# Performance work log

Measured on AMD Instinct MI355X. Metric: run time of the kernel, lower is better.

## Reference

```python
import jax, jax.numpy as jnp
import numpy as np

N = 50000      # nodes
E = 800000     # edges (avg degree 16)
EMB = 128      # emb_dim
NF = 7         # x_features
EF = 5         # edge_features
L = 5          # num_layer
BN_EPS = 1e-5


def setup_inputs() -> dict:
    key = jax.random.key(0)
    ks = jax.random.split(key, 12)
    s = 0.05
    return {
        "x": jax.random.normal(ks[0], (N, NF), jnp.float32),
        "edge_attr": jax.random.normal(ks[1], (E, EF), jnp.float32),
        "edge_index": jax.random.randint(ks[2], (2, E), 0, N, dtype=jnp.int32),
        "W_x": jax.random.normal(ks[3], (NF, EMB), jnp.float32) * s,
        "b_x": jax.random.normal(ks[4], (NF, EMB), jnp.float32) * s,
        "W_e": jax.random.normal(ks[5], (L, EF, EMB), jnp.float32) * s,
        "b_e": jax.random.normal(ks[6], (L, EF, EMB), jnp.float32) * s,
        # per-layer GIN update MLP: Linear(EMB,2EMB)-ReLU-Linear(2EMB,EMB)
        "W1": jax.random.normal(ks[7], (L, EMB, 2 * EMB), jnp.float32) * s,
        "b1": jnp.zeros((L, 2 * EMB), jnp.float32),
        "W2": jax.random.normal(ks[8], (L, 2 * EMB, EMB), jnp.float32) * s,
        "b2": jnp.zeros((L, EMB), jnp.float32),
        # per-layer BatchNorm1d affine params
        "gamma": jnp.ones((L, EMB), jnp.float32),
        "beta": jnp.zeros((L, EMB), jnp.float32),
    }


def reference(x, edge_attr, W_x, b_x, W_e, b_e, W1, b1, W2, b2, gamma, beta, edge_index):
    src, dst = edge_index[0], edge_index[1]
    # initial node embedding: sum of 7 Linear(1,EMB) applied per column == x @ W_x + sum(biases)
    h = x @ W_x + b_x.sum(axis=0)  # [N, EMB]
    for l in range(L):
        # edge embeddings: sum of EF Linear(1,EMB) over edge_attr columns
        e_emb = edge_attr @ W_e[l] + b_e[l].sum(axis=0)  # [E, EMB]
        sl_emb = b_e[l].sum(axis=0)  # self-loop edges have zero attr -> bias sum
        # message = x_j + edge_emb, aggr = add (scatter over dst); self loops add h + sl_emb
        msg = h[src] + e_emb                                        # [E, EMB]
        agg = jax.ops.segment_sum(msg, dst, num_segments=N) + h + sl_emb  # [N, EMB]
        # GIN update MLP
        z = jax.nn.relu(agg @ W1[l] + b1[l]) @ W2[l] + b2[l]        # [N, EMB]
        # BatchNorm1d (training-mode batch stats, biased variance)
        mu = z.mean(axis=0)
        var = z.var(axis=0)
        z = (z - mu) * jax.lax.rsqrt(var + BN_EPS) * gamma[l] + beta[l]
        # ELU on all but last layer; dropout is identity at drop_ratio=0; JK='last'
        h = jax.nn.elu(z) if l < L - 1 else z
    return h
```

## Files before the change

kernel.cpp:

```cpp
#include <hip/hip_runtime.h>
#include <math.h>

#define NN 50000
#define NE 800000
#define EMB 128
#define HID 256
#define NF 7
#define EF 5
#define NL 5
#define BN_EPS 1e-5f
#define NREP 32
#define SCAN_B 196
#define NBUCK 49

typedef _Float16 f16x8 __attribute__((ext_vector_type(8)));
typedef _Float16 f16x2 __attribute__((ext_vector_type(2)));
typedef __attribute__((ext_vector_type(4))) float f32x4;

__device__ inline unsigned pkh2(float a, float b) {
    union { unsigned v; _Float16 h[2]; } x;
    x.h[0] = (_Float16)a; x.h[1] = (_Float16)b;
    return x.v;
}
__device__ inline float2 uph2(unsigned u) {
    union { unsigned v; _Float16 h[2]; } x; x.v = u;
    return make_float2((float)x.h[0], (float)x.h[1]);
}
__device__ inline unsigned short f2h_bits(float f) {
    _Float16 h = (_Float16)f;
    return __builtin_bit_cast(unsigned short, h);
}
__device__ inline float h_bits2f(unsigned short b) {
    return (float)__builtin_bit_cast(_Float16, b);
}
__device__ inline f16x2 as_h2(unsigned u) { return __builtin_bit_cast(f16x2, u); }

__global__ void k_prep(const float* __restrict__ b_x, const float* __restrict__ b_e,
                       float* __restrict__ bsum_x, float* __restrict__ bsum_e,
                       int* __restrict__ counts, int* __restrict__ cursor) {
    int tid = threadIdx.x;
    if (blockIdx.x == 0 && tid < EMB) {
        float s = 0.f;
        for (int f = 0; f < NF; ++f) s += b_x[f * EMB + tid];
        bsum_x[tid] = s;
        for (int l = 0; l < NL; ++l) {
            float se = 0.f;
            for (int f = 0; f < EF; ++f) se += b_e[(l * EF + f) * EMB + tid];
            bsum_e[l * EMB + tid] = se;
        }
    }
    int gid = blockIdx.x * blockDim.x + tid;
    int stride = gridDim.x * blockDim.x;
    for (int i = gid; i < NN; i += stride) { counts[i] = 0; cursor[i] = 0; }
}

__global__ void k_prepw(const float* __restrict__ W1, const float* __restrict__ W2,
                        unsigned short* __restrict__ W1ph, unsigned short* __restrict__ W1pl,
                        unsigned short* __restrict__ W2ph, unsigned short* __restrict__ W2pl) {
    const int TOT = NL * EMB * HID;
    int gid = blockIdx.x * blockDim.x + threadIdx.x;
    if (gid < TOT) {
        int l = gid / (EMB * HID);
        int r = gid % (EMB * HID);
        int w = r >> 13;
        int rem = r & 8191;
        int h2 = rem >> 11;
        int rem2 = rem & 2047;
        int kk = rem2 >> 9;
        int rem3 = rem2 & 511;
        int lane = rem3 >> 3;
        int j = rem3 & 7;
        int hc = w * 64 + h2 * 16 + (lane & 15);
        int k = kk * 32 + (lane >> 4) * 8 + j;
        float wv = W1[((size_t)l * EMB + k) * HID + hc];
        unsigned short hi = f2h_bits(wv);
        W1ph[gid] = hi;
        W1pl[gid] = f2h_bits(wv - h_bits2f(hi));
    } else if (gid < 2 * TOT) {
        int g = gid - TOT;
        int l = g / (EMB * HID);
        int r = g % (EMB * HID);
        int w = r >> 13;
        int rem = r & 8191;
        int o2 = rem >> 12;
        int rem2 = rem & 4095;
        int kk = rem2 >> 9;
        int rem3 = rem2 & 511;
        int lane = rem3 >> 3;
        int j = rem3 & 7;
        int oc = w * 32 + o2 * 16 + (lane & 15);
        int k2 = kk * 32 + (lane >> 4) * 8 + j;
        float wv = W2[((size_t)l * HID + k2) * EMB + oc];
        unsigned short hi = f2h_bits(wv);
        W2ph[g] = hi;
        W2pl[g] = f2h_bits(wv - h_bits2f(hi));
    }
}

__global__ void k_init(const float* __restrict__ x, const float* __restrict__ W_x,
                       const float* __restrict__ bsum_x, unsigned short* __restrict__ h16) {
    int gid = blockIdx.x * blockDim.x + threadIdx.x;
    int v = gid >> 5;
    if (v >= NN) return;
    int c = (gid & 31) << 2;
    float4 acc = *(const float4*)(bsum_x + c);
    #pragma unroll
    for (int f = 0; f < NF; ++f) {
        float xv = x[(size_t)v * NF + f];
        float4 w = *(const float4*)(W_x + f * EMB + c);
        acc.x += xv * w.x; acc.y += xv * w.y; acc.z += xv * w.z; acc.w += xv * w.w;
    }
    uint2 p = make_uint2(pkh2(acc.x, acc.y), pkh2(acc.z, acc.w));
    *(uint2*)(h16 + (size_t)v * EMB + c) = p;
}

__global__ void k_hist(const int* __restrict__ dst, int* __restrict__ counts) {
    int e = blockIdx.x * blockDim.x + threadIdx.x;
    if (e < NE) atomicAdd(&counts[dst[e]], 1);
}

__global__ void k_scan1(const int* __restrict__ counts, int* __restrict__ bsum) {
    int tid = threadIdx.x;
    int i = blockIdx.x * 256 + tid;
    int v = (i < NN) ? counts[i] : 0;
    #pragma unroll
    for (int off = 1; off < 64; off <<= 1) v += __shfl_xor(v, off, 64);
    __shared__ int ws[4];
    if ((tid & 63) == 0) ws[tid >> 6] = v;
    __syncthreads();
    if (tid == 0) bsum[blockIdx.x] = ws[0] + ws[1] + ws[2] + ws[3];
}

__global__ void k_scan2(const int* __restrict__ bsum, int* __restrict__ bpre,
                        int* __restrict__ row_start) {
    int tid = threadIdx.x;
    int x = (tid < SCAN_B) ? bsum[tid] : 0;
    int lane = tid & 63, wv = tid >> 6;
    int v = x;
    #pragma unroll
    for (int off = 1; off < 64; off <<= 1) {
        int t = __shfl_up(v, off, 64);
        if (lane >= off) v += t;
    }
    __shared__ int wsum[4];
    if (lane == 63) wsum[wv] = v;
    __syncthreads();
    int woff = 0;
    #pragma unroll
    for (int w = 0; w < 4; ++w) if (w < wv) woff += wsum[w];
    int incl = v + woff;
    if (tid < SCAN_B) bpre[tid] = incl - x;
    if (tid == 255) row_start[NN] = incl;
}

__global__ void k_scan3(const int* __restrict__ counts, const int* __restrict__ bpre,
                        int* __restrict__ row_start, int* __restrict__ bcur) {
    int tid = threadIdx.x;
    int i = blockIdx.x * 256 + tid;
    int x = (i < NN) ? counts[i] : 0;
    int lane = tid & 63, wv = tid >> 6;
    int v = x;
    #pragma unroll
    for (int off = 1; off < 64; off <<= 1) {
        int t = __shfl_up(v, off, 64);
        if (lane >= off) v += t;
    }
    __shared__ int wsum[4];
    if (lane == 63) wsum[wv] = v;
    __syncthreads();
    int woff = 0;
    #pragma unroll
    for (int w = 0; w < 4; ++w) if (w < wv) woff += wsum[w];
    if (i < NN) {
        int rs = bpre[blockIdx.x] + v + woff - x;
        row_start[i] = rs;
        if ((i & 1023) == 0) bcur[i >> 10] = rs;
    }
}

#define BPB 2048
__global__ __launch_bounds__(256) void k_bucket(
        const int* __restrict__ src, const int* __restrict__ dst,
        const float* __restrict__ edge_attr,
        int* __restrict__ bcur, uint4* __restrict__ grouped) {
    __shared__ int lcnt[NBUCK];
    __shared__ int lbase[NBUCK];
    int tid = threadIdx.x;
    if (tid < NBUCK) lcnt[tid] = 0;
    __syncthreads();
    int base = blockIdx.x * BPB;
    int b_[8];
    int d_[8];
    #pragma unroll
    for (int k = 0; k < 8; ++k) {
        int e = base + k * 256 + tid;
        if (e < NE) {
            int d = dst[e];
            d_[k] = d;
            b_[k] = d >> 10;
            atomicAdd(&lcnt[b_[k]], 1);
        } else b_[k] = -1;
    }
    __syncthreads();
    if (tid < NBUCK) {
        lbase[tid] = (lcnt[tid] > 0) ? atomicAdd(&bcur[tid], lcnt[tid]) : 0;
        lcnt[tid] = 0;
    }
    __syncthreads();
    #pragma unroll
    for (int k = 0; k < 8; ++k) {
        int e = base + k * 256 + tid;
        if (e < NE) {
            int b = b_[k];
            int off = lbase[b] + atomicAdd(&lcnt[b], 1);
            const float* ea = edge_attr + (size_t)e * EF;
            uint4 pk;
            pk.x = (unsigned)src[e];
            pk.y = pkh2(ea[0], ea[1]);
            pk.z = pkh2(ea[2], ea[3]);
            pk.w = (unsigned)f2h_bits(ea[4]) | ((unsigned)d_[k] << 16);
            grouped[off] = pk;
        }
    }
}

__global__ void k_place(const uint4* __restrict__ grouped,
                        const int* __restrict__ row_start, int* __restrict__ cursor,
                        uint4* __restrict__ sorted_pk) {
    int e = blockIdx.x * blockDim.x + threadIdx.x;
    if (e >= NE) return;
    uint4 pk = grouped[e];
    int d = (int)(pk.w >> 16);
    int pos = atomicAdd(&cursor[d], 1);
    sorted_pk[row_start[d] + pos] = pk;
}

__global__ void k_esum(const uint4* __restrict__ sorted_pk,
                       const int* __restrict__ row_start,
                       float* __restrict__ attsum, int* __restrict__ sorted_srcc) {
    int v = blockIdx.x * blockDim.x + threadIdx.x;
    if (v >= NN) return;
    int e0 = row_start[v], e1 = row_start[v + 1];
    float s0 = 0.f, s1 = 0.f, s2 = 0.f, s3 = 0.f, s4 = 0.f;
    for (int e = e0; e < e1; ++e) {
        uint4 pk = sorted_pk[e];
        sorted_srcc[e] = (int)pk.x;
        float2 a01 = uph2(pk.y), a23 = uph2(pk.z);
        s0 += a01.x; s1 += a01.y; s2 += a23.x; s3 += a23.y;
        s4 += h_bits2f((unsigned short)(pk.w & 0xffffu));
    }
    float* o = attsum + (size_t)v * 8;
    *(float4*)(o) = make_float4(s0, s1, s2, s3);
    *(float4*)(o + 4) = make_float4(s4, (float)(e1 - e0), 0.f, 0.f);
}

__global__ __launch_bounds__(256) void k_agg(
        const unsigned short* __restrict__ h16, const int* __restrict__ sorted_srcc,
        const float* __restrict__ attsum,
        const float* __restrict__ W_e_l, const float* __restrict__ bsum_e_l,
        const int* __restrict__ row_start,
        unsigned short* __restrict__ agg16, float* __restrict__ stats) {
    int tid = threadIdx.x;
    if (blockIdx.x < NREP) stats[blockIdx.x * 2 * EMB + tid] = 0.f;
    int gid = blockIdx.x * 256 + tid;
    int v = gid >> 6;
    if (v >= NN) return;
    int c = (gid & 63) << 1;
    float2 we0 = *(const float2*)(W_e_l + 0 * EMB + c);
    float2 we1 = *(const float2*)(W_e_l + 1 * EMB + c);
    float2 we2 = *(const float2*)(W_e_l + 2 * EMB + c);
    float2 we3 = *(const float2*)(W_e_l + 3 * EMB + c);
    float2 we4 = *(const float2*)(W_e_l + 4 * EMB + c);
    float2 bs = *(const float2*)(bsum_e_l + c);
    float2 hv = uph2(*(const unsigned*)(h16 + (size_t)v * EMB + c));
    const float* at = attsum + (size_t)v * 8;
    float4 a03 = *(const float4*)(at);
    float2 a45 = *(const float2*)(at + 4);
    float ax = hv.x + (a45.y + 1.f) * bs.x
             + a03.x*we0.x + a03.y*we1.x + a03.z*we2.x + a03.w*we3.x + a45.x*we4.x;
    float ay = hv.y + (a45.y + 1.f) * bs.y
             + a03.x*we0.y + a03.y*we1.y + a03.z*we2.y + a03.w*we3.y + a45.x*we4.y;
    int e0 = row_start[v], e1 = row_start[v + 1];
    int e = e0;
    for (; e + 16 <= e1; e += 16) {
        int s0 = __builtin_amdgcn_readfirstlane(sorted_srcc[e + 0]);
        int s1 = __builtin_amdgcn_readfirstlane(sorted_srcc[e + 1]);
        int s2 = __builtin_amdgcn_readfirstlane(sorted_srcc[e + 2]);
        int s3 = __builtin_amdgcn_readfirstlane(sorted_srcc[e + 3]);
        int s4 = __builtin_amdgcn_readfirstlane(sorted_srcc[e + 4]);
        int s5 = __builtin_amdgcn_readfirstlane(sorted_srcc[e + 5]);
        int s6 = __builtin_amdgcn_readfirstlane(sorted_srcc[e + 6]);
        int s7 = __builtin_amdgcn_readfirstlane(sorted_srcc[e + 7]);
        int s8 = __builtin_amdgcn_readfirstlane(sorted_srcc[e + 8]);
        int s9 = __builtin_amdgcn_readfirstlane(sorted_srcc[e + 9]);
        int sa = __builtin_amdgcn_readfirstlane(sorted_srcc[e + 10]);
        int sb = __builtin_amdgcn_readfirstlane(sorted_srcc[e + 11]);
        int sc = __builtin_amdgcn_readfirstlane(sorted_srcc[e + 12]);
        int sd = __builtin_amdgcn_readfirstlane(sorted_srcc[e + 13]);
        int se = __builtin_amdgcn_readfirstlane(sorted_srcc[e + 14]);
        int sf = __builtin_amdgcn_readfirstlane(sorted_srcc[e + 15]);
        unsigned u0 = *(const unsigned*)(h16 + (size_t)s0 * EMB + c);
        unsigned u1 = *(const unsigned*)(h16 + (size_t)s1 * EMB + c);
        unsigned u2 = *(const unsigned*)(h16 + (size_t)s2 * EMB + c);
        unsigned u3 = *(const unsigned*)(h16 + (size_t)s3 * EMB + c);
        unsigned u4 = *(const unsigned*)(h16 + (size_t)s4 * EMB + c);
        unsigned u5 = *(const unsigned*)(h16 + (size_t)s5 * EMB + c);
        unsigned u6 = *(const unsigned*)(h16 + (size_t)s6 * EMB + c);
        unsigned u7 = *(const unsigned*)(h16 + (size_t)s7 * EMB + c);
        unsigned u8 = *(const unsigned*)(h16 + (size_t)s8 * EMB + c);
        unsigned u9 = *(const unsigned*)(h16 + (size_t)s9 * EMB + c);
        unsigned ua = *(const unsigned*)(h16 + (size_t)sa * EMB + c);
        unsigned ub = *(const unsigned*)(h16 + (size_t)sb * EMB + c);
        unsigned uc = *(const unsigned*)(h16 + (size_t)sc * EMB + c);
        unsigned ud = *(const unsigned*)(h16 + (size_t)sd * EMB + c);
        unsigned ue = *(const unsigned*)(h16 + (size_t)se * EMB + c);
        unsigned uf = *(const unsigned*)(h16 + (size_t)sf * EMB + c);
        f16x2 pA = ((as_h2(u0) + as_h2(u1)) + (as_h2(u2) + as_h2(u3)))
                 + ((as_h2(u4) + as_h2(u5)) + (as_h2(u6) + as_h2(u7)));
        f16x2 pB = ((as_h2(u8) + as_h2(u9)) + (as_h2(ua) + as_h2(ub)))
                 + ((as_h2(uc) + as_h2(ud)) + (as_h2(ue) + as_h2(uf)));
        ax += (float)pA.x + (float)pB.x;
        ay += (float)pA.y + (float)pB.y;
    }
    for (; e + 8 <= e1; e += 8) {
        int s0 = __builtin_amdgcn_readfirstlane(sorted_srcc[e + 0]);
        int s1 = __builtin_amdgcn_readfirstlane(sorted_srcc[e + 1]);
        int s2 = __builtin_amdgcn_readfirstlane(sorted_srcc[e + 2]);
        int s3 = __builtin_amdgcn_readfirstlane(sorted_srcc[e + 3]);
        int s4 = __builtin_amdgcn_readfirstlane(sorted_srcc[e + 4]);
        int s5 = __builtin_amdgcn_readfirstlane(sorted_srcc[e + 5]);
        int s6 = __builtin_amdgcn_readfirstlane(sorted_srcc[e + 6]);
        int s7 = __builtin_amdgcn_readfirstlane(sorted_srcc[e + 7]);
        unsigned u0 = *(const unsigned*)(h16 + (size_t)s0 * EMB + c);
        unsigned u1 = *(const unsigned*)(h16 + (size_t)s1 * EMB + c);
        unsigned u2 = *(const unsigned*)(h16 + (size_t)s2 * EMB + c);
        unsigned u3 = *(const unsigned*)(h16 + (size_t)s3 * EMB + c);
        unsigned u4 = *(const unsigned*)(h16 + (size_t)s4 * EMB + c);
        unsigned u5 = *(const unsigned*)(h16 + (size_t)s5 * EMB + c);
        unsigned u6 = *(const unsigned*)(h16 + (size_t)s6 * EMB + c);
        unsigned u7 = *(const unsigned*)(h16 + (size_t)s7 * EMB + c);
        f16x2 p07 = ((as_h2(u0) + as_h2(u1)) + (as_h2(u2) + as_h2(u3)))
                  + ((as_h2(u4) + as_h2(u5)) + (as_h2(u6) + as_h2(u7)));
        ax += (float)p07.x;
        ay += (float)p07.y;
    }
    for (; e < e1; ++e) {
        int s = __builtin_amdgcn_readfirstlane(sorted_srcc[e]);
        float2 hs = uph2(*(const unsigned*)(h16 + (size_t)s * EMB + c));
        ax += hs.x;
        ay += hs.y;
    }
    *(unsigned*)(agg16 + (size_t)v * EMB + c) = pkh2(ax, ay);
}

__global__ __launch_bounds__(256) void k_mlp(
        const unsigned short* __restrict__ agg16,
        const unsigned short* __restrict__ W1ph, const unsigned short* __restrict__ W1pl,
        const float* __restrict__ b1_l,
        const unsigned short* __restrict__ W2ph, const unsigned short* __restrict__ W2pl,
        const float* __restrict__ b2_l,
        unsigned short* __restrict__ z16, float* __restrict__ stats) {
    __shared__ unsigned short A16[64][136];
    __shared__ unsigned short Hid16[64][264];
    int tid = threadIdx.x;
    int r0 = blockIdx.x * 64;
    int rep = blockIdx.x & (NREP - 1);
    #pragma unroll
    for (int it = 0; it < 4; ++it) {
        int idx = it * 256 + tid;
        int row = idx >> 4;
        int cb = (idx & 15) * 8;
        int grow = r0 + row;
        uint4 val = make_uint4(0u, 0u, 0u, 0u);
        if (grow < NN) val = *(const uint4*)(agg16 + (size_t)grow * EMB + cb);
        *(uint4*)(&A16[row][cb]) = val;
    }
    __syncthreads();
    int wave = tid >> 6, lane = tid & 63;
    int l16 = lane & 15, quad = lane >> 4;
    {
        f16x8 af[4][4];
        #pragma unroll
        for (int nt = 0; nt < 4; ++nt)
            #pragma unroll
            for (int kk = 0; kk < 4; ++kk)
                af[nt][kk] = *(const f16x8*)(&A16[nt * 16 + l16][kk * 32 + quad * 8]);
        #pragma unroll
        for (int h2 = 0; h2 < 4; ++h2) {
            f16x8 whf[4], wlf[4];
            #pragma unroll
            for (int kk = 0; kk < 4; ++kk) {
                size_t off = ((((size_t)(wave * 4 + h2) * 4) + kk) * 64 + lane) * 8;
                whf[kk] = *(const f16x8*)(W1ph + off);
                wlf[kk] = *(const f16x8*)(W1pl + off);
            }
            float4 bv = *(const float4*)(b1_l + wave * 64 + h2 * 16 + quad * 4);
            f32x4 bias = {bv.x, bv.y, bv.z, bv.w};
            #pragma unroll
            for (int nt = 0; nt < 4; ++nt) {
                f32x4 acc = bias;
                #pragma unroll
                for (int kk = 0; kk < 4; ++kk)
                    acc = __builtin_amdgcn_mfma_f32_16x16x32_f16(whf[kk], af[nt][kk], acc, 0, 0, 0);
                #pragma unroll
                for (int kk = 0; kk < 4; ++kk)
                    acc = __builtin_amdgcn_mfma_f32_16x16x32_f16(wlf[kk], af[nt][kk], acc, 0, 0, 0);
                uint2 p;
                p.x = pkh2(fmaxf(acc[0], 0.f), fmaxf(acc[1], 0.f));
                p.y = pkh2(fmaxf(acc[2], 0.f), fmaxf(acc[3], 0.f));
                int col = wave * 64 + h2 * 16 + quad * 4;
                *(uint2*)(&Hid16[nt * 16 + l16][col]) = p;
            }
        }
    }
    __syncthreads();
    float ss[2][4] = {}, sq[2][4] = {};
    #pragma unroll
    for (int o2 = 0; o2 < 2; ++o2) {
        f16x8 w2h[8], w2l[8];
        #pragma unroll
        for (int kk = 0; kk < 8; ++kk) {
            size_t off = ((((size_t)(wave * 2 + o2) * 8) + kk) * 64 + lane) * 8;
            w2h[kk] = *(const f16x8*)(W2ph + off);
            w2l[kk] = *(const f16x8*)(W2pl + off);
        }
        float4 bv = *(const float4*)(b2_l + wave * 32 + o2 * 16 + quad * 4);
        f32x4 bias = {bv.x, bv.y, bv.z, bv.w};
        #pragma unroll
        for (int nt = 0; nt < 4; ++nt) {
            f16x8 hf[8];
            #pragma unroll
            for (int kk = 0; kk < 8; ++kk)
                hf[kk] = *(const f16x8*)(&Hid16[nt * 16 + l16][kk * 32 + quad * 8]);
            f32x4 acc = bias;
            #pragma unroll
            for (int kk = 0; kk < 8; ++kk)
                acc = __builtin_amdgcn_mfma_f32_16x16x32_f16(w2h[kk], hf[kk], acc, 0, 0, 0);
            #pragma unroll
            for (int kk = 0; kk < 8; ++kk)
                acc = __builtin_amdgcn_mfma_f32_16x16x32_f16(w2l[kk], hf[kk], acc, 0, 0, 0);
            int node = r0 + nt * 16 + l16;
            if (node < NN) {
                uint2 p = make_uint2(pkh2(acc[0], acc[1]), pkh2(acc[2], acc[3]));
                *(uint2*)(z16 + (size_t)node * EMB + wave * 32 + o2 * 16 + quad * 4) = p;
                #pragma unroll
                for (int r = 0; r < 4; ++r) {
                    ss[o2][r] += acc[r];
                    sq[o2][r] += acc[r] * acc[r];
                }
            }
        }
    }
    #pragma unroll
    for (int o2 = 0; o2 < 2; ++o2)
        #pragma unroll
        for (int r = 0; r < 4; ++r) {
            float s = ss[o2][r], q = sq[o2][r];
            #pragma unroll
            for (int m = 1; m < 16; m <<= 1) {
                s += __shfl_xor(s, m, 64);
                q += __shfl_xor(q, m, 64);
            }
            if (l16 == 0) {
                int oc = wave * 32 + o2 * 16 + quad * 4 + r;
                atomicAdd(&stats[rep * 2 * EMB + oc], s);
                atomicAdd(&stats[rep * 2 * EMB + EMB + oc], q);
            }
        }
}

__global__ void k_bnscale(const float* __restrict__ stats,
                          const float* __restrict__ gamma_l, const float* __restrict__ beta_l,
                          float* __restrict__ scsh) {
    int tid = threadIdx.x;
    float s = 0.f, q = 0.f;
    #pragma unroll
    for (int r = 0; r < NREP; ++r) {
        s += stats[r * 2 * EMB + tid];
        q += stats[r * 2 * EMB + EMB + tid];
    }
    float mu = s * (1.f / NN);
    float var = q * (1.f / NN) - mu * mu;
    float sf = gamma_l[tid] * rsqrtf(var + BN_EPS);
    scsh[tid] = sf;
    scsh[EMB + tid] = beta_l[tid] - mu * sf;
}

__global__ void k_bn(const unsigned short* __restrict__ z16, const float* __restrict__ scsh,
                     unsigned short* __restrict__ h16, float* __restrict__ fout, int last) {
    __shared__ float sc[EMB], sh[EMB];
    int tid = threadIdx.x;
    if (tid < EMB) {
        sc[tid] = scsh[tid];
        sh[tid] = scsh[EMB + tid];
    }
    __syncthreads();
    int gid = blockIdx.x * blockDim.x + tid;
    if (gid >= NN * EMB / 4) return;
    int c = (gid & 31) << 2;
    uint2 zp = *(const uint2*)(z16 + (size_t)gid * 4);
    float2 z01 = uph2(zp.x), z23 = uph2(zp.y);
    float o0 = z01.x * sc[c + 0] + sh[c + 0];
    float o1 = z01.y * sc[c + 1] + sh[c + 1];
    float o2 = z23.x * sc[c + 2] + sh[c + 2];
    float o3 = z23.y * sc[c + 3] + sh[c + 3];
    if (!last) {
        o0 = (o0 > 0.f) ? o0 : (__expf(o0) - 1.f);
        o1 = (o1 > 0.f) ? o1 : (__expf(o1) - 1.f);
        o2 = (o2 > 0.f) ? o2 : (__expf(o2) - 1.f);
        o3 = (o3 > 0.f) ? o3 : (__expf(o3) - 1.f);
        uint2 p = make_uint2(pkh2(o0, o1), pkh2(o2, o3));
        *(uint2*)(h16 + (size_t)gid * 4) = p;
    } else {
        *(float4*)(fout + (size_t)gid * 4) = make_float4(o0, o1, o2, o3);
    }
}

extern "C" void kernel_launch(void* const* d_in, const int* in_sizes, int n_in,
                              void* d_out, int out_size, void* d_ws, size_t ws_size,
                              hipStream_t stream) {
    const float* x         = (const float*)d_in[0];
    const float* edge_attr = (const float*)d_in[1];
    const int*   edge_idx  = (const int*)d_in[2];
    const float* W_x   = (const float*)d_in[3];
    const float* b_x   = (const float*)d_in[4];
    const float* W_e   = (const float*)d_in[5];
    const float* b_e   = (const float*)d_in[6];
    const float* W1    = (const float*)d_in[7];
    const float* b1    = (const float*)d_in[8];
    const float* W2    = (const float*)d_in[9];
    const float* b2    = (const float*)d_in[10];
    const float* gamma = (const float*)d_in[11];
    const float* beta  = (const float*)d_in[12];
    float* fout = (float*)d_out;

    const int* src = edge_idx;
    const int* dst = edge_idx + NE;

    char* p = (char*)d_ws;
    auto alloc = [&](size_t bytes) { char* q = p; p += (bytes + 255) & ~(size_t)255; return q; };
    unsigned short* h16  = (unsigned short*)alloc((size_t)NN * EMB * 2);
    unsigned short* z16  = (unsigned short*)alloc((size_t)NN * EMB * 2);
    unsigned short* agg16 = (unsigned short*)alloc((size_t)NN * EMB * 2);
    unsigned short* W1ph = (unsigned short*)alloc((size_t)NL * HID * EMB * 2);
    unsigned short* W1pl = (unsigned short*)alloc((size_t)NL * HID * EMB * 2);
    unsigned short* W2ph = (unsigned short*)alloc((size_t)NL * EMB * HID * 2);
    unsigned short* W2pl = (unsigned short*)alloc((size_t)NL * EMB * HID * 2);
    int*   row_start  = (int*)alloc((NN + 1) * sizeof(int));
    int*   counts     = (int*)alloc(NN * sizeof(int));
    int*   cursor     = (int*)alloc(NN * sizeof(int));
    uint4* grouped    = (uint4*)alloc((size_t)NE * sizeof(uint4));
    uint4* sorted_pk  = (uint4*)alloc((size_t)NE * sizeof(uint4));
    int*   sorted_srcc= (int*)alloc((size_t)NE * sizeof(int));
    float* attsum     = (float*)alloc((size_t)NN * 8 * sizeof(float));
    int*   bsum       = (int*)alloc(SCAN_B * sizeof(int));
    int*   bpre       = (int*)alloc(SCAN_B * sizeof(int));
    int*   bcur       = (int*)alloc(NBUCK * sizeof(int));
    float* stats      = (float*)alloc((size_t)NREP * 2 * EMB * sizeof(float));
    float* scsh       = (float*)alloc(2 * EMB * sizeof(float));
    float* bsum_x     = (float*)alloc(EMB * sizeof(float));
    float* bsum_e     = (float*)alloc(NL * EMB * sizeof(float));

    k_prep<<<256, 256, 0, stream>>>(b_x, b_e, bsum_x, bsum_e, counts, cursor);
    k_prepw<<<(2 * NL * EMB * HID + 255) / 256, 256, 0, stream>>>(W1, W2, W1ph, W1pl, W2ph, W2pl);
    k_init<<<(NN * 32 + 255) / 256, 256, 0, stream>>>(x, W_x, bsum_x, h16);
    k_hist<<<(NE + 255) / 256, 256, 0, stream>>>(dst, counts);
    k_scan1<<<SCAN_B, 256, 0, stream>>>(counts, bsum);
    k_scan2<<<1, 256, 0, stream>>>(bsum, bpre, row_start);
    k_scan3<<<SCAN_B, 256, 0, stream>>>(counts, bpre, row_start, bcur);
    k_bucket<<<(NE + BPB - 1) / BPB, 256, 0, stream>>>(src, dst, edge_attr, bcur, grouped);
    k_place<<<(NE + 255) / 256, 256, 0, stream>>>(grouped, row_start, cursor, sorted_pk);
    k_esum<<<SCAN_B, 256, 0, stream>>>(sorted_pk, row_start, attsum, sorted_srcc);
    const int AGG_GRID = (NN * 64 + 255) / 256;
    for (int l = 0; l < NL; ++l) {
        k_agg<<<AGG_GRID, 256, 0, stream>>>(
            h16, sorted_srcc, attsum,
            W_e + (size_t)l * EF * EMB, bsum_e + l * EMB, row_start,
            agg16, stats);
        k_mlp<<<(NN + 63) / 64, 256, 0, stream>>>(
            agg16,
            W1ph + (size_t)l * HID * EMB, W1pl + (size_t)l * HID * EMB, b1 + (size_t)l * HID,
            W2ph + (size_t)l * EMB * HID, W2pl + (size_t)l * EMB * HID, b2 + (size_t)l * EMB,
            z16, stats);
        k_bnscale<<<1, 128, 0, stream>>>(stats, gamma + l * EMB, beta + l * EMB, scsh);
        k_bn<<<(NN * EMB / 4 + 255) / 256, 256, 0, stream>>>(
            z16, scsh, h16, fout, (l == NL - 1) ? 1 : 0);
    }
}
```

Measured before the change: 572.2 us.

## Fuse neighbor aggregation into MLP kernel and merge BN scale into BN apply

```diff
diff --git a/kernel.cpp b/kernel.cpp
--- a/kernel.cpp
+++ b/kernel.cpp
@@ -37,7 +37,8 @@
 
 __global__ void k_prep(const float* __restrict__ b_x, const float* __restrict__ b_e,
                        float* __restrict__ bsum_x, float* __restrict__ bsum_e,
-                       int* __restrict__ counts, int* __restrict__ cursor) {
+                       int* __restrict__ counts, int* __restrict__ cursor,
+                       float* __restrict__ stats) {
     int tid = threadIdx.x;
     if (blockIdx.x == 0 && tid < EMB) {
         float s = 0.f;
@@ -52,6 +53,8 @@
     int gid = blockIdx.x * blockDim.x + tid;
     int stride = gridDim.x * blockDim.x;
     for (int i = gid; i < NN; i += stride) { counts[i] = 0; cursor[i] = 0; }
+    const int STOT = NL * NREP * 2 * EMB;
+    for (int i = gid; i < STOT; i += stride) stats[i] = 0.f;
 }
 
 __global__ void k_prepw(const float* __restrict__ W1, const float* __restrict__ W2,
@@ -254,129 +257,119 @@
     *(float4*)(o + 4) = make_float4(s4, (float)(e1 - e0), 0.f, 0.f);
 }
 
-__global__ __launch_bounds__(256) void k_agg(
+__global__ __launch_bounds__(256) void k_fused(
         const unsigned short* __restrict__ h16, const int* __restrict__ sorted_srcc,
         const float* __restrict__ attsum,
         const float* __restrict__ W_e_l, const float* __restrict__ bsum_e_l,
         const int* __restrict__ row_start,
-        unsigned short* __restrict__ agg16, float* __restrict__ stats) {
-    int tid = threadIdx.x;
-    if (blockIdx.x < NREP) stats[blockIdx.x * 2 * EMB + tid] = 0.f;
-    int gid = blockIdx.x * 256 + tid;
-    int v = gid >> 6;
-    if (v >= NN) return;
-    int c = (gid & 63) << 1;
-    float2 we0 = *(const float2*)(W_e_l + 0 * EMB + c);
-    float2 we1 = *(const float2*)(W_e_l + 1 * EMB + c);
-    float2 we2 = *(const float2*)(W_e_l + 2 * EMB + c);
-    float2 we3 = *(const float2*)(W_e_l + 3 * EMB + c);
-    float2 we4 = *(const float2*)(W_e_l + 4 * EMB + c);
-    float2 bs = *(const float2*)(bsum_e_l + c);
-    float2 hv = uph2(*(const unsigned*)(h16 + (size_t)v * EMB + c));
-    const float* at = attsum + (size_t)v * 8;
-    float4 a03 = *(const float4*)(at);
-    float2 a45 = *(const float2*)(at + 4);
-    float ax = hv.x + (a45.y + 1.f) * bs.x
-             + a03.x*we0.x + a03.y*we1.x + a03.z*we2.x + a03.w*we3.x + a45.x*we4.x;
-    float ay = hv.y + (a45.y + 1.f) * bs.y
-             + a03.x*we0.y + a03.y*we1.y + a03.z*we2.y + a03.w*we3.y + a45.x*we4.y;
-    int e0 = row_start[v], e1 = row_start[v + 1];
-    int e = e0;
-    for (; e + 16 <= e1; e += 16) {
-        int s0 = __builtin_amdgcn_readfirstlane(sorted_srcc[e + 0]);
-        int s1 = __builtin_amdgcn_readfirstlane(sorted_srcc[e + 1]);
-        int s2 = __builtin_amdgcn_readfirstlane(sorted_srcc[e + 2]);
-        int s3 = __builtin_amdgcn_readfirstlane(sorted_srcc[e + 3]);
-        int s4 = __builtin_amdgcn_readfirstlane(sorted_srcc[e + 4]);
-        int s5 = __builtin_amdgcn_readfirstlane(sorted_srcc[e + 5]);
-        int s6 = __builtin_amdgcn_readfirstlane(sorted_srcc[e + 6]);
-        int s7 = __builtin_amdgcn_readfirstlane(sorted_srcc[e + 7]);
-        int s8 = __builtin_amdgcn_readfirstlane(sorted_srcc[e + 8]);
-        int s9 = __builtin_amdgcn_readfirstlane(sorted_srcc[e + 9]);
-        int sa = __builtin_amdgcn_readfirstlane(sorted_srcc[e + 10]);
-        int sb = __builtin_amdgcn_readfirstlane(sorted_srcc[e + 11]);
-        int sc = __builtin_amdgcn_readfirstlane(sorted_srcc[e + 12]);
-        int sd = __builtin_amdgcn_readfirstlane(sorted_srcc[e + 13]);
-        int se = __builtin_amdgcn_readfirstlane(sorted_srcc[e + 14]);
-        int sf = __builtin_amdgcn_readfirstlane(sorted_srcc[e + 15]);
-        unsigned u0 = *(const unsigned*)(h16 + (size_t)s0 * EMB + c);
-        unsigned u1 = *(const unsigned*)(h16 + (size_t)s1 * EMB + c);
-        unsigned u2 = *(const unsigned*)(h16 + (size_t)s2 * EMB + c);
-        unsigned u3 = *(const unsigned*)(h16 + (size_t)s3 * EMB + c);
-        unsigned u4 = *(const unsigned*)(h16 + (size_t)s4 * EMB + c);
-        unsigned u5 = *(const unsigned*)(h16 + (size_t)s5 * EMB + c);
-        unsigned u6 = *(const unsigned*)(h16 + (size_t)s6 * EMB + c);
-        unsigned u7 = *(const unsigned*)(h16 + (size_t)s7 * EMB + c);
-        unsigned u8 = *(const unsigned*)(h16 + (size_t)s8 * EMB + c);
-        unsigned u9 = *(const unsigned*)(h16 + (size_t)s9 * EMB + c);
-        unsigned ua = *(const unsigned*)(h16 + (size_t)sa * EMB + c);
-        unsigned ub = *(const unsigned*)(h16 + (size_t)sb * EMB + c);
-        unsigned uc = *(const unsigned*)(h16 + (size_t)sc * EMB + c);
-        unsigned ud = *(const unsigned*)(h16 + (size_t)sd * EMB + c);
-        unsigned ue = *(const unsigned*)(h16 + (size_t)se * EMB + c);
-        unsigned uf = *(const unsigned*)(h16 + (size_t)sf * EMB + c);
-        f16x2 pA = ((as_h2(u0) + as_h2(u1)) + (as_h2(u2) + as_h2(u3)))
-                 + ((as_h2(u4) + as_h2(u5)) + (as_h2(u6) + as_h2(u7)));
-        f16x2 pB = ((as_h2(u8) + as_h2(u9)) + (as_h2(ua) + as_h2(ub)))
-                 + ((as_h2(uc) + as_h2(ud)) + (as_h2(ue) + as_h2(uf)));
-        ax += (float)pA.x + (float)pB.x;
-        ay += (float)pA.y + (float)pB.y;
-    }
-    for (; e + 8 <= e1; e += 8) {
-        int s0 = __builtin_amdgcn_readfirstlane(sorted_srcc[e + 0]);
-        int s1 = __builtin_amdgcn_readfirstlane(sorted_srcc[e + 1]);
-        int s2 = __builtin_amdgcn_readfirstlane(sorted_srcc[e + 2]);
-        int s3 = __builtin_amdgcn_readfirstlane(sorted_srcc[e + 3]);
-        int s4 = __builtin_amdgcn_readfirstlane(sorted_srcc[e + 4]);
-        int s5 = __builtin_amdgcn_readfirstlane(sorted_srcc[e + 5]);
-        int s6 = __builtin_amdgcn_readfirstlane(sorted_srcc[e + 6]);
-        int s7 = __builtin_amdgcn_readfirstlane(sorted_srcc[e + 7]);
-        unsigned u0 = *(const unsigned*)(h16 + (size_t)s0 * EMB + c);
-        unsigned u1 = *(const unsigned*)(h16 + (size_t)s1 * EMB + c);
-        unsigned u2 = *(const unsigned*)(h16 + (size_t)s2 * EMB + c);
-        unsigned u3 = *(const unsigned*)(h16 + (size_t)s3 * EMB + c);
-        unsigned u4 = *(const unsigned*)(h16 + (size_t)s4 * EMB + c);
-        unsigned u5 = *(const unsigned*)(h16 + (size_t)s5 * EMB + c);
-        unsigned u6 = *(const unsigned*)(h16 + (size_t)s6 * EMB + c);
-        unsigned u7 = *(const unsigned*)(h16 + (size_t)s7 * EMB + c);
-        f16x2 p07 = ((as_h2(u0) + as_h2(u1)) + (as_h2(u2) + as_h2(u3)))
-                  + ((as_h2(u4) + as_h2(u5)) + (as_h2(u6) + as_h2(u7)));
-        ax += (float)p07.x;
-        ay += (float)p07.y;
-    }
-    for (; e < e1; ++e) {
-        int s = __builtin_amdgcn_readfirstlane(sorted_srcc[e]);
-        float2 hs = uph2(*(const unsigned*)(h16 + (size_t)s * EMB + c));
-        ax += hs.x;
-        ay += hs.y;
-    }
-    *(unsigned*)(agg16 + (size_t)v * EMB + c) = pkh2(ax, ay);
-}
-
-__global__ __launch_bounds__(256) void k_mlp(
-        const unsigned short* __restrict__ agg16,
         const unsigned short* __restrict__ W1ph, const unsigned short* __restrict__ W1pl,
         const float* __restrict__ b1_l,
         const unsigned short* __restrict__ W2ph, const unsigned short* __restrict__ W2pl,
         const float* __restrict__ b2_l,
-        unsigned short* __restrict__ z16, float* __restrict__ stats) {
+        unsigned short* __restrict__ z16, float* __restrict__ stats_l) {
     __shared__ unsigned short A16[64][136];
     __shared__ unsigned short Hid16[64][264];
     int tid = threadIdx.x;
+    int wave = tid >> 6, lane = tid & 63;
     int r0 = blockIdx.x * 64;
     int rep = blockIdx.x & (NREP - 1);
-    #pragma unroll
-    for (int it = 0; it < 4; ++it) {
-        int idx = it * 256 + tid;
-        int row = idx >> 4;
-        int cb = (idx & 15) * 8;
-        int grow = r0 + row;
-        uint4 val = make_uint4(0u, 0u, 0u, 0u);
-        if (grow < NN) val = *(const uint4*)(agg16 + (size_t)grow * EMB + cb);
-        *(uint4*)(&A16[row][cb]) = val;
-    }
-    __syncthreads();
-    int wave = tid >> 6, lane = tid & 63;
+
+    {
+        int c = lane << 1;
+        float2 we0 = *(const float2*)(W_e_l + 0 * EMB + c);
+        float2 we1 = *(const float2*)(W_e_l + 1 * EMB + c);
+        float2 we2 = *(const float2*)(W_e_l + 2 * EMB + c);
+        float2 we3 = *(const float2*)(W_e_l + 3 * EMB + c);
+        float2 we4 = *(const float2*)(W_e_l + 4 * EMB + c);
+        float2 bs = *(const float2*)(bsum_e_l + c);
+        for (int i = 0; i < 16; ++i) {
+            int v = r0 + wave * 16 + i;
+            unsigned out = 0u;
+            if (v < NN) {
+                float2 hv = uph2(*(const unsigned*)(h16 + (size_t)v * EMB + c));
+                const float* at = attsum + (size_t)v * 8;
+                float4 a03 = *(const float4*)(at);
+                float2 a45 = *(const float2*)(at + 4);
+                float ax = hv.x + (a45.y + 1.f) * bs.x
+                         + a03.x*we0.x + a03.y*we1.x + a03.z*we2.x + a03.w*we3.x + a45.x*we4.x;
+                float ay = hv.y + (a45.y + 1.f) * bs.y
+                         + a03.x*we0.y + a03.y*we1.y + a03.z*we2.y + a03.w*we3.y + a45.x*we4.y;
+                int e0 = row_start[v], e1 = row_start[v + 1];
+                int e = e0;
+                for (; e + 16 <= e1; e += 16) {
+                    int s0 = __builtin_amdgcn_readfirstlane(sorted_srcc[e + 0]);
+                    int s1 = __builtin_amdgcn_readfirstlane(sorted_srcc[e + 1]);
+                    int s2 = __builtin_amdgcn_readfirstlane(sorted_srcc[e + 2]);
+                    int s3 = __builtin_amdgcn_readfirstlane(sorted_srcc[e + 3]);
+                    int s4 = __builtin_amdgcn_readfirstlane(sorted_srcc[e + 4]);
+                    int s5 = __builtin_amdgcn_readfirstlane(sorted_srcc[e + 5]);
+                    int s6 = __builtin_amdgcn_readfirstlane(sorted_srcc[e + 6]);
+                    int s7 = __builtin_amdgcn_readfirstlane(sorted_srcc[e + 7]);
+                    int s8 = __builtin_amdgcn_readfirstlane(sorted_srcc[e + 8]);
+                    int s9 = __builtin_amdgcn_readfirstlane(sorted_srcc[e + 9]);
+                    int sa = __builtin_amdgcn_readfirstlane(sorted_srcc[e + 10]);
+                    int sb = __builtin_amdgcn_readfirstlane(sorted_srcc[e + 11]);
+                    int sc = __builtin_amdgcn_readfirstlane(sorted_srcc[e + 12]);
+                    int sd = __builtin_amdgcn_readfirstlane(sorted_srcc[e + 13]);
+                    int se = __builtin_amdgcn_readfirstlane(sorted_srcc[e + 14]);
+                    int sf = __builtin_amdgcn_readfirstlane(sorted_srcc[e + 15]);
+                    unsigned u0 = *(const unsigned*)(h16 + (size_t)s0 * EMB + c);
+                    unsigned u1 = *(const unsigned*)(h16 + (size_t)s1 * EMB + c);
+                    unsigned u2 = *(const unsigned*)(h16 + (size_t)s2 * EMB + c);
+                    unsigned u3 = *(const unsigned*)(h16 + (size_t)s3 * EMB + c);
+                    unsigned u4 = *(const unsigned*)(h16 + (size_t)s4 * EMB + c);
+                    unsigned u5 = *(const unsigned*)(h16 + (size_t)s5 * EMB + c);
+                    unsigned u6 = *(const unsigned*)(h16 + (size_t)s6 * EMB + c);
+                    unsigned u7 = *(const unsigned*)(h16 + (size_t)s7 * EMB + c);
+                    unsigned u8 = *(const unsigned*)(h16 + (size_t)s8 * EMB + c);
+                    unsigned u9 = *(const unsigned*)(h16 + (size_t)s9 * EMB + c);
+                    unsigned ua = *(const unsigned*)(h16 + (size_t)sa * EMB + c);
+                    unsigned ub = *(const unsigned*)(h16 + (size_t)sb * EMB + c);
+                    unsigned uc = *(const unsigned*)(h16 + (size_t)sc * EMB + c);
+                    unsigned ud = *(const unsigned*)(h16 + (size_t)sd * EMB + c);
+                    unsigned ue = *(const unsigned*)(h16 + (size_t)se * EMB + c);
+                    unsigned uf = *(const unsigned*)(h16 + (size_t)sf * EMB + c);
+                    f16x2 pA = ((as_h2(u0) + as_h2(u1)) + (as_h2(u2) + as_h2(u3)))
+                             + ((as_h2(u4) + as_h2(u5)) + (as_h2(u6) + as_h2(u7)));
+                    f16x2 pB = ((as_h2(u8) + as_h2(u9)) + (as_h2(ua) + as_h2(ub)))
+                             + ((as_h2(uc) + as_h2(ud)) + (as_h2(ue) + as_h2(uf)));
+                    ax += (float)pA.x + (float)pB.x;
+                    ay += (float)pA.y + (float)pB.y;
+                }
+                for (; e + 8 <= e1; e += 8) {
+                    int s0 = __builtin_amdgcn_readfirstlane(sorted_srcc[e + 0]);
+                    int s1 = __builtin_amdgcn_readfirstlane(sorted_srcc[e + 1]);
+                    int s2 = __builtin_amdgcn_readfirstlane(sorted_srcc[e + 2]);
+                    int s3 = __builtin_amdgcn_readfirstlane(sorted_srcc[e + 3]);
+                    int s4 = __builtin_amdgcn_readfirstlane(sorted_srcc[e + 4]);
+                    int s5 = __builtin_amdgcn_readfirstlane(sorted_srcc[e + 5]);
+                    int s6 = __builtin_amdgcn_readfirstlane(sorted_srcc[e + 6]);
+                    int s7 = __builtin_amdgcn_readfirstlane(sorted_srcc[e + 7]);
+                    unsigned u0 = *(const unsigned*)(h16 + (size_t)s0 * EMB + c);
+                    unsigned u1 = *(const unsigned*)(h16 + (size_t)s1 * EMB + c);
+                    unsigned u2 = *(const unsigned*)(h16 + (size_t)s2 * EMB + c);
+                    unsigned u3 = *(const unsigned*)(h16 + (size_t)s3 * EMB + c);
+                    unsigned u4 = *(const unsigned*)(h16 + (size_t)s4 * EMB + c);
+                    unsigned u5 = *(const unsigned*)(h16 + (size_t)s5 * EMB + c);
+                    unsigned u6 = *(const unsigned*)(h16 + (size_t)s6 * EMB + c);
+                    unsigned u7 = *(const unsigned*)(h16 + (size_t)s7 * EMB + c);
+                    f16x2 p07 = ((as_h2(u0) + as_h2(u1)) + (as_h2(u2) + as_h2(u3)))
+                              + ((as_h2(u4) + as_h2(u5)) + (as_h2(u6) + as_h2(u7)));
+                    ax += (float)p07.x;
+                    ay += (float)p07.y;
+                }
+                for (; e < e1; ++e) {
+                    int s = __builtin_amdgcn_readfirstlane(sorted_srcc[e]);
+                    float2 hs = uph2(*(const unsigned*)(h16 + (size_t)s * EMB + c));
+                    ax += hs.x;
+                    ay += hs.y;
+                }
+                out = pkh2(ax, ay);
+            }
+            *(unsigned*)(&A16[wave * 16 + i][c]) = out;
+        }
+    }
+    __syncthreads();
     int l16 = lane & 15, quad = lane >> 4;
     {
         f16x8 af[4][4];
@@ -463,56 +456,54 @@
             }
             if (l16 == 0) {
                 int oc = wave * 32 + o2 * 16 + quad * 4 + r;
-                atomicAdd(&stats[rep * 2 * EMB + oc], s);
-                atomicAdd(&stats[rep * 2 * EMB + EMB + oc], q);
+                atomicAdd(&stats_l[rep * 2 * EMB + oc], s);
+                atomicAdd(&stats_l[rep * 2 * EMB + EMB + oc], q);
             }
         }
 }
 
-__global__ void k_bnscale(const float* __restrict__ stats,
+__global__ void k_bnfused(const float* __restrict__ stats_l,
                           const float* __restrict__ gamma_l, const float* __restrict__ beta_l,
-                          float* __restrict__ scsh) {
-    int tid = threadIdx.x;
-    float s = 0.f, q = 0.f;
-    #pragma unroll
-    for (int r = 0; r < NREP; ++r) {
-        s += stats[r * 2 * EMB + tid];
-        q += stats[r * 2 * EMB + EMB + tid];
-    }
-    float mu = s * (1.f / NN);
-    float var = q * (1.f / NN) - mu * mu;
-    float sf = gamma_l[tid] * rsqrtf(var + BN_EPS);
-    scsh[tid] = sf;
-    scsh[EMB + tid] = beta_l[tid] - mu * sf;
-}
-
-__global__ void k_bn(const unsigned short* __restrict__ z16, const float* __restrict__ scsh,
-                     unsigned short* __restrict__ h16, float* __restrict__ fout, int last) {
+                          const unsigned short* __restrict__ z16,
+                          unsigned short* __restrict__ h16, float* __restrict__ fout, int last) {
+    __shared__ float red[2 * EMB];
     __shared__ float sc[EMB], sh[EMB];
     int tid = threadIdx.x;
+    {
+        float acc = 0.f;
+        #pragma unroll
+        for (int r = 0; r < NREP; ++r) acc += stats_l[r * 2 * EMB + tid];
+        red[tid] = acc;
+    }
+    __syncthreads();
     if (tid < EMB) {
-        sc[tid] = scsh[tid];
-        sh[tid] = scsh[EMB + tid];
-    }
-    __syncthreads();
-    int gid = blockIdx.x * blockDim.x + tid;
-    if (gid >= NN * EMB / 4) return;
-    int c = (gid & 31) << 2;
-    uint2 zp = *(const uint2*)(z16 + (size_t)gid * 4);
-    float2 z01 = uph2(zp.x), z23 = uph2(zp.y);
-    float o0 = z01.x * sc[c + 0] + sh[c + 0];
-    float o1 = z01.y * sc[c + 1] + sh[c + 1];
-    float o2 = z23.x * sc[c + 2] + sh[c + 2];
-    float o3 = z23.y * sc[c + 3] + sh[c + 3];
-    if (!last) {
-        o0 = (o0 > 0.f) ? o0 : (__expf(o0) - 1.f);
-        o1 = (o1 > 0.f) ? o1 : (__expf(o1) - 1.f);
-        o2 = (o2 > 0.f) ? o2 : (__expf(o2) - 1.f);
-        o3 = (o3 > 0.f) ? o3 : (__expf(o3) - 1.f);
-        uint2 p = make_uint2(pkh2(o0, o1), pkh2(o2, o3));
-        *(uint2*)(h16 + (size_t)gid * 4) = p;
-    } else {
-        *(float4*)(fout + (size_t)gid * 4) = make_float4(o0, o1, o2, o3);
+        float s = red[tid], q = red[EMB + tid];
+        float mu = s * (1.f / NN);
+        float var = q * (1.f / NN) - mu * mu;
+        float sf = gamma_l[tid] * rsqrtf(var + BN_EPS);
+        sc[tid] = sf;
+        sh[tid] = beta_l[tid] - mu * sf;
+    }
+    __syncthreads();
+    const int TOT = NN * EMB / 4;
+    for (int gid = blockIdx.x * 256 + tid; gid < TOT; gid += gridDim.x * 256) {
+        int c = (gid & 31) << 2;
+        uint2 zp = *(const uint2*)(z16 + (size_t)gid * 4);
+        float2 z01 = uph2(zp.x), z23 = uph2(zp.y);
+        float o0 = z01.x * sc[c + 0] + sh[c + 0];
+        float o1 = z01.y * sc[c + 1] + sh[c + 1];
+        float o2 = z23.x * sc[c + 2] + sh[c + 2];
+        float o3 = z23.y * sc[c + 3] + sh[c + 3];
+        if (!last) {
+            o0 = (o0 > 0.f) ? o0 : (__expf(o0) - 1.f);
+            o1 = (o1 > 0.f) ? o1 : (__expf(o1) - 1.f);
+            o2 = (o2 > 0.f) ? o2 : (__expf(o2) - 1.f);
+            o3 = (o3 > 0.f) ? o3 : (__expf(o3) - 1.f);
+            uint2 p = make_uint2(pkh2(o0, o1), pkh2(o2, o3));
+            *(uint2*)(h16 + (size_t)gid * 4) = p;
+        } else {
+            *(float4*)(fout + (size_t)gid * 4) = make_float4(o0, o1, o2, o3);
+        }
     }
 }
 
@@ -541,7 +532,6 @@
     auto alloc = [&](size_t bytes) { char* q = p; p += (bytes + 255) & ~(size_t)255; return q; };
     unsigned short* h16  = (unsigned short*)alloc((size_t)NN * EMB * 2);
     unsigned short* z16  = (unsigned short*)alloc((size_t)NN * EMB * 2);
-    unsigned short* agg16 = (unsigned short*)alloc((size_t)NN * EMB * 2);
     unsigned short* W1ph = (unsigned short*)alloc((size_t)NL * HID * EMB * 2);
     unsigned short* W1pl = (unsigned short*)alloc((size_t)NL * HID * EMB * 2);
     unsigned short* W2ph = (unsigned short*)alloc((size_t)NL * EMB * HID * 2);
@@ -556,12 +546,11 @@
     int*   bsum       = (int*)alloc(SCAN_B * sizeof(int));
     int*   bpre       = (int*)alloc(SCAN_B * sizeof(int));
     int*   bcur       = (int*)alloc(NBUCK * sizeof(int));
-    float* stats      = (float*)alloc((size_t)NREP * 2 * EMB * sizeof(float));
-    float* scsh       = (float*)alloc(2 * EMB * sizeof(float));
+    float* stats      = (float*)alloc((size_t)NL * NREP * 2 * EMB * sizeof(float));
     float* bsum_x     = (float*)alloc(EMB * sizeof(float));
     float* bsum_e     = (float*)alloc(NL * EMB * sizeof(float));
 
-    k_prep<<<256, 256, 0, stream>>>(b_x, b_e, bsum_x, bsum_e, counts, cursor);
+    k_prep<<<256, 256, 0, stream>>>(b_x, b_e, bsum_x, bsum_e, counts, cursor, stats);
     k_prepw<<<(2 * NL * EMB * HID + 255) / 256, 256, 0, stream>>>(W1, W2, W1ph, W1pl, W2ph, W2pl);
     k_init<<<(NN * 32 + 255) / 256, 256, 0, stream>>>(x, W_x, bsum_x, h16);
     k_hist<<<(NE + 255) / 256, 256, 0, stream>>>(dst, counts);
@@ -571,19 +560,15 @@
     k_bucket<<<(NE + BPB - 1) / BPB, 256, 0, stream>>>(src, dst, edge_attr, bcur, grouped);
     k_place<<<(NE + 255) / 256, 256, 0, stream>>>(grouped, row_start, cursor, sorted_pk);
     k_esum<<<SCAN_B, 256, 0, stream>>>(sorted_pk, row_start, attsum, sorted_srcc);
-    const int AGG_GRID = (NN * 64 + 255) / 256;
     for (int l = 0; l < NL; ++l) {
-        k_agg<<<AGG_GRID, 256, 0, stream>>>(
+        float* stats_l = stats + (size_t)l * NREP * 2 * EMB;
+        k_fused<<<(NN + 63) / 64, 256, 0, stream>>>(
             h16, sorted_srcc, attsum,
             W_e + (size_t)l * EF * EMB, bsum_e + l * EMB, row_start,
-            agg16, stats);
-        k_mlp<<<(NN + 63) / 64, 256, 0, stream>>>(
-            agg16,
             W1ph + (size_t)l * HID * EMB, W1pl + (size_t)l * HID * EMB, b1 + (size_t)l * HID,
             W2ph + (size_t)l * EMB * HID, W2pl + (size_t)l * EMB * HID, b2 + (size_t)l * EMB,
-            z16, stats);
-        k_bnscale<<<1, 128, 0, stream>>>(stats, gamma + l * EMB, beta + l * EMB, scsh);
-        k_bn<<<(NN * EMB / 4 + 255) / 256, 256, 0, stream>>>(
-            z16, scsh, h16, fout, (l == NL - 1) ? 1 : 0);
-    }
-}
+            z16, stats_l);
+        k_bnfused<<<2048, 256, 0, stream>>>(
+            stats_l, gamma + l * EMB, beta + l * EMB, z16, h16, fout, (l == NL - 1) ? 1 : 0);
+    }
+}
```

Result: slower. 857.3 us (+49.8%).
